# Performance work log

Hardware: AMD Instinct MI355X
Metric: run time of the kernel (lower is better)

The kernel has to match this reference:

```python
import jax, jax.numpy as jnp
import numpy as np

EMB = 128
BINS = 32
CUT = 5.0
NLAYER = 5
NHID = 4  # extra hidden linears in edge MLP (hidden_dim_list has 5 entries total)
N_NODES = 50000
N_EDGES = 800000
N_GRAPH = 256
NODE_CLASS = 100


def setup_inputs() -> dict:
    key = jax.random.key(0)
    ks = jax.random.split(key, 20)
    s = 0.02
    inp = {
        'z': jax.random.randint(ks[0], (N_NODES,), 0, NODE_CLASS),
        'pos': jax.random.normal(ks[1], (N_NODES, 3), dtype=jnp.float32) * 3.0,
        'batch': jnp.sort(jax.random.randint(ks[2], (N_NODES,), 0, N_GRAPH)),
        'edge_index': jax.random.randint(ks[3], (2, N_EDGES), 0, N_NODES),
        # parameters
        'atom_table': jax.random.normal(ks[4], (NODE_CLASS, EMB), dtype=jnp.float32) * s,
        'atom_w': jax.random.normal(ks[5], (EMB, EMB), dtype=jnp.float32) * s,
        'atom_b': jnp.zeros((EMB,), jnp.float32),
        'edge_emb_w': jax.random.normal(ks[6], (BINS, EMB), dtype=jnp.float32) * s,
        'edge_emb_b': jnp.zeros((EMB,), jnp.float32),
        'edge_w0': jax.random.normal(ks[7], (NLAYER, 3 * EMB, EMB), dtype=jnp.float32) * s,
        'edge_b0': jnp.zeros((NLAYER, EMB), jnp.float32),
        'edge_w': jax.random.normal(ks[8], (NLAYER, NHID, EMB, EMB), dtype=jnp.float32) * s,
        'edge_b': jnp.zeros((NLAYER, NHID, EMB), jnp.float32),
        'node_w': jax.random.normal(ks[9], (NLAYER, EMB, EMB), dtype=jnp.float32) * s,
        'node_b': jnp.zeros((NLAYER, EMB), jnp.float32),
        'out_w': jax.random.normal(ks[10], (EMB, 1), dtype=jnp.float32) * s,
        'out_b': jnp.zeros((1,), jnp.float32),
    }
    return inp


def reference(z, pos, batch, edge_index, atom_table, atom_w, atom_b,
              edge_emb_w, edge_emb_b, edge_w0, edge_b0, edge_w, edge_b,
              node_w, node_b, out_w, out_b):
    silu = jax.nn.silu
    row, col = edge_index[0], edge_index[1]

    # atom embedding + linear
    h_node = atom_table[z] @ atom_w + atom_b  # [N, EMB]

    # edge distances -> gaussian basis expansion (linear spacing, log_base=1.0)
    d = jnp.linalg.norm(pos[row] - pos[col], axis=-1)  # [E]
    mu = jnp.linspace(0.0, CUT, BINS, dtype=jnp.float32)
    sigma = CUT / BINS
    basis = jnp.exp(-0.5 * ((d[:, None] - mu) / sigma) ** 2)  # [E, BINS]
    h_edge = basis @ edge_emb_w + edge_emb_b  # [E, EMB]

    # message passing layers
    for l in range(NLAYER):
        m = jnp.concatenate([h_edge, h_node[row], h_node[col]], axis=-1)  # [E, 3*EMB]
        m = silu(m @ edge_w0[l] + edge_b0[l])
        for k in range(NHID):
            m = silu(m @ edge_w[l, k] + edge_b[l, k])
        h_edge = h_edge + m  # residual edge update
        agg = jax.ops.segment_sum(h_edge, row, num_segments=N_NODES)  # [N, EMB]
        h_node = h_node + silu(agg @ node_w[l] + node_b[l])  # residual node update

    # scatter-mean graph pool
    sums = jax.ops.segment_sum(h_node, batch, num_segments=N_GRAPH)
    cnt = jax.ops.segment_sum(jnp.ones((h_node.shape[0],), h_node.dtype), batch, num_segments=N_GRAPH)
    h_graph = sums / jnp.clip(cnt, 1.0)[:, None]

    return h_graph @ out_w + out_b  # [N_GRAPH, 1]
```

## Files before the change

kernel.cpp:

```cpp
#include <hip/hip_runtime.h>

#define EMB      128
#define N_NODES_ 50000
#define N_EDGES_ 800000
#define N_GRAPH_ 256
#define NLAYER_  5

#define WP_ATOM  573440
#define WP_NODE0 589824
#define WP_EMB   671744
#define WP_TOTAL 675840

typedef short short8 __attribute__((ext_vector_type(8)));
typedef float floatx4 __attribute__((ext_vector_type(4)));
typedef unsigned uintx2 __attribute__((ext_vector_type(2)));

__device__ __forceinline__ float silu_f(float x) {
    return __fdividef(x, 1.0f + __expf(-x));
}
__device__ __forceinline__ float bf2f(unsigned short h) {
    return __uint_as_float(((unsigned)h) << 16);
}
__device__ __forceinline__ unsigned short f2bf(float f) {
    unsigned u = __float_as_uint(f);
    unsigned r = 0x7FFFu + ((u >> 16) & 1u);
    return (unsigned short)((u + r) >> 16);
}

#if defined(__has_builtin)
#if __has_builtin(__builtin_amdgcn_cvt_pk_bf16_f32)
#define HAVE_PK_BF16 1
#endif
#if __has_builtin(__builtin_amdgcn_permlane16_swap) && __has_builtin(__builtin_amdgcn_permlane32_swap)
#define HAVE_PERMLANE_SWAP 1
#endif
#endif

#ifdef HAVE_PK_BF16
typedef __bf16 bf16x2 __attribute__((ext_vector_type(2)));
__device__ __forceinline__ unsigned f2bf_pk(float a, float b) {
    bf16x2 v = __builtin_amdgcn_cvt_pk_bf16_f32(a, b);
    unsigned u;
    __builtin_memcpy(&u, &v, 4);
    return u;
}
#else
__device__ __forceinline__ unsigned f2bf_pk(float a, float b) {
    return (unsigned)f2bf(a) | ((unsigned)f2bf(b) << 16);
}
#endif

__device__ __forceinline__ void wave_lds_fence() {
    __builtin_amdgcn_fence(__ATOMIC_ACQ_REL, "wavefront");
    __builtin_amdgcn_wave_barrier();
}

__device__ __forceinline__ void gload_lds16(const unsigned short* g, unsigned short* l) {
    __builtin_amdgcn_global_load_lds(
        (const __attribute__((address_space(1))) void*)g,
        (__attribute__((address_space(3))) void*)l,
        16, 0, 0);
}

__device__ __forceinline__ void swap32(unsigned &a, unsigned &b) {
#ifdef HAVE_PERMLANE_SWAP
    uintx2 r = __builtin_amdgcn_permlane32_swap(a, b, false, false);
    a = r.x; b = r.y;
#else
    const int lane = (int)(threadIdx.x & 63);
    const int idx = (lane ^ 32) << 2;
    const unsigned ta = (unsigned)__builtin_amdgcn_ds_bpermute(idx, (int)a);
    const unsigned tb = (unsigned)__builtin_amdgcn_ds_bpermute(idx, (int)b);
    const bool hi = lane >= 32;
    const unsigned na = hi ? tb : a;
    const unsigned nb = hi ? b : ta;
    a = na; b = nb;
#endif
}
__device__ __forceinline__ void swap16(unsigned &a, unsigned &b) {
#ifdef HAVE_PERMLANE_SWAP
    uintx2 r = __builtin_amdgcn_permlane16_swap(a, b, false, false);
    a = r.x; b = r.y;
#else
    const unsigned ta = (unsigned)__builtin_amdgcn_ds_swizzle((int)a, 0x401F);
    const unsigned tb = (unsigned)__builtin_amdgcn_ds_swizzle((int)b, 0x401F);
    const bool odd = ((threadIdx.x >> 4) & 1) != 0;
    const unsigned na = odd ? tb : a;
    const unsigned nb = odd ? b : ta;
    a = na; b = nb;
#endif
}

__device__ __forceinline__ short8 xchg_frag(uint2 pkE, uint2 pkO) {
    unsigned a0 = pkE.x, b0 = pkO.x;
    unsigned a1 = pkE.y, b1 = pkO.y;
    swap32(a0, b0); swap16(a0, b0);
    swap32(a1, b1); swap16(a1, b1);
    union { short8 s; unsigned u[4]; } r;
    r.u[0] = a0; r.u[1] = a1; r.u[2] = b0; r.u[3] = b1;
    return r.s;
}

__device__ __forceinline__ floatx4 upair_sum(uint2 a, uint2 b) {
    floatx4 r;
    r[0] = bf2f((unsigned short)(a.x & 0xFFFF)) + bf2f((unsigned short)(b.x & 0xFFFF));
    r[1] = bf2f((unsigned short)(a.x >> 16))    + bf2f((unsigned short)(b.x >> 16));
    r[2] = bf2f((unsigned short)(a.y & 0xFFFF)) + bf2f((unsigned short)(b.y & 0xFFFF));
    r[3] = bf2f((unsigned short)(a.y >> 16))    + bf2f((unsigned short)(b.y >> 16));
    return r;
}

__global__ __launch_bounds__(256) void hist_kernel(
    const int* __restrict__ row, int* __restrict__ hist)
{
    const int e = blockIdx.x * 256 + threadIdx.x;
    if (e < N_EDGES_) atomicAdd(&hist[row[e]], 1);
}

__global__ __launch_bounds__(256) void scan_kernel(
    const int* __restrict__ hist, int* __restrict__ cursor)
{
    __shared__ int ssum[256];
    const int tid = threadIdx.x;
    const int chunk = (N_NODES_ + 255) / 256;
    const int base = tid * chunk;
    int s = 0;
    for (int i = 0; i < chunk; ++i) {
        const int idx = base + i;
        if (idx < N_NODES_) s += hist[idx];
    }
    ssum[tid] = s;
    __syncthreads();
    for (int off = 1; off < 256; off <<= 1) {
        const int t2 = (tid >= off) ? ssum[tid - off] : 0;
        __syncthreads();
        ssum[tid] += t2;
        __syncthreads();
    }
    int run = ssum[tid] - s;
    for (int i = 0; i < chunk; ++i) {
        const int idx = base + i;
        if (idx < N_NODES_) { cursor[idx] = run; run += hist[idx]; }
    }
}

__global__ __launch_bounds__(256) void scatter_kernel(
    const int* __restrict__ row, const int* __restrict__ col,
    int* __restrict__ cursor, int* __restrict__ row_s, int* __restrict__ col_s)
{
    const int e = blockIdx.x * 256 + threadIdx.x;
    if (e >= N_EDGES_) return;
    const int r = row[e];
    const int p = atomicAdd(&cursor[r], 1);
    row_s[p] = r;
    col_s[p] = col[e];
}

__global__ __launch_bounds__(256) void pack_w_kernel(
    const float* __restrict__ edge_w0, const float* __restrict__ edge_w,
    const float* __restrict__ atom_w, const float* __restrict__ node_w,
    const float* __restrict__ edge_emb_w,
    unsigned short* __restrict__ Wp)
{
    const int bid = blockIdx.x;
    int Kb, t;
    const float* src;
    unsigned short* dst;
    if (bid < 200) {
        const int l = bid / 40, r = bid % 40, s = r / 8;
        t = r % 8;
        Kb = (s == 0) ? 12 : 4;
        src = (s == 0) ? edge_w0 + (size_t)l * 384 * 128
                       : edge_w + ((size_t)l * 4 + (s - 1)) * 128 * 128;
        dst = Wp + (size_t)l * 114688 + ((s == 0) ? 0 : (49152 + (s - 1) * 16384))
            + (size_t)t * Kb * 512;
    } else if (bid < 208) {
        t = bid - 200; Kb = 4; src = atom_w;
        dst = Wp + WP_ATOM + (size_t)t * Kb * 512;
    } else if (bid < 248) {
        const int l = (bid - 208) >> 3; t = (bid - 208) & 7; Kb = 4;
        src = node_w + (size_t)l * 128 * 128;
        dst = Wp + WP_NODE0 + (size_t)l * 16384 + (size_t)t * Kb * 512;
    } else {
        t = bid - 248; Kb = 1; src = edge_emb_w;
        dst = Wp + WP_EMB + (size_t)t * 512;
    }
    const int n = Kb * 512;
    for (int p = threadIdx.x; p < n; p += 256) {
        const int j = p & 7, lane = (p >> 3) & 63, kb = p >> 9;
        const int k  = kb * 32 + ((lane >> 4) << 3) + j;
        const int nn = t * 16 + (lane & 15);
        dst[p] = f2bf(src[(size_t)k * 128 + nn]);
    }
}

__global__ __launch_bounds__(128, 5) void edge_mlp_csr_kernel(
    unsigned short* __restrict__ h_edge,
    const unsigned short* __restrict__ Ur, const unsigned short* __restrict__ Uc,
    const int* __restrict__ row_s, const int* __restrict__ col_s,
    const unsigned short* __restrict__ Wp, const float* __restrict__ bh)
{
    __shared__ __align__(16) unsigned short Xs[4096];
    __shared__ __align__(16) unsigned short Ys[4096];

    const int tid  = threadIdx.x;
    const int lane = tid & 63;
    const int wv   = tid >> 6;
    const int lr   = lane & 15;
    const int lg   = lane >> 4;
    const int e0   = blockIdx.x * 32;
    const int ntb  = 4 * wv;

    const int srow = 16 * wv + lg;
#pragma unroll
    for (int j = 0; j < 4; ++j) {
        const int r = srow + 4 * j;
        const int c = lr ^ (r & 7);
        gload_lds16(h_edge + (size_t)(e0 + r) * 128 + c * 8,
                    &Xs[(16 * wv + 4 * j) * 128]);
    }

    int rid[2], cid[2];
#pragma unroll
    for (int et = 0; et < 2; ++et) {
        const int e = e0 + et * 16 + lr;
        rid[et] = row_s[e];
        cid[et] = col_s[e];
    }

    floatx4 acc[2][4];
    {
        uint2 gr[2][4], gc[2][4];
#pragma unroll
        for (int et = 0; et < 2; ++et)
#pragma unroll
            for (int n = 0; n < 4; ++n) {
                const int fo = (ntb + n) * 16 + lg * 4;
                gr[et][n] = *(const uint2*)(Ur + (size_t)rid[et] * 128 + fo);
                gc[et][n] = *(const uint2*)(Uc + (size_t)cid[et] * 128 + fo);
            }
#pragma unroll
        for (int et = 0; et < 2; ++et)
#pragma unroll
            for (int n = 0; n < 4; ++n)
                acc[et][n] = upair_sum(gr[et][n], gc[et][n]);
    }

    asm volatile("s_waitcnt vmcnt(0)" ::: "memory");
    __syncthreads();

    short8 he_reg[4];
    const int t_ = tid >> 2, q_ = tid & 3;

#pragma unroll 1
    for (int s = 0; s < 5; ++s) {
        const unsigned short* __restrict__ bin = (s & 1) ? Ys : Xs;
        unsigned short* __restrict__ bout      = (s & 1) ? Xs : Ys;
        const unsigned short* __restrict__ Ws =
            (s == 0) ? Wp : (Wp + 49152 + (size_t)(s - 1) * 16384);
        const int nst = (s == 0) ? 12 : 4;

        if (s >= 1) {
            const float* bias = bh + (size_t)(s - 1) * 128;
#pragma unroll
            for (int n = 0; n < 4; ++n) {
                const float4 bv = *(const float4*)&bias[(ntb + n) * 16 + lg * 4];
                acc[0][n] = (floatx4){bv.x, bv.y, bv.z, bv.w};
                acc[1][n] = acc[0][n];
            }
        }

#pragma unroll 2
        for (int kk = 0; kk < 4; ++kk) {
            short8 wf[4];
#pragma unroll
            for (int n = 0; n < 4; ++n)
                wf[n] = *(const short8*)(Ws + ((size_t)((ntb + n) * nst + kk) * 64 + lane) * 8);
#pragma unroll
            for (int et = 0; et < 2; ++et) {
                const int r = et * 16 + lr;
                const short8 mf = *(const short8*)&bin[r * 128 + (((kk * 4 + lg) ^ (r & 7)) << 3)];
#pragma unroll
                for (int n = 0; n < 4; ++n)
                    acc[et][n] = __builtin_amdgcn_mfma_f32_16x16x32_bf16(wf[n], mf, acc[et][n], 0, 0, 0);
            }
        }

#pragma unroll
        for (int et = 0; et < 2; ++et) {
            const int r = et * 16 + lr;
#pragma unroll
            for (int n = 0; n < 4; ++n) {
                uint2 p;
                p.x = f2bf_pk(silu_f(acc[et][n][0]), silu_f(acc[et][n][1]));
                p.y = f2bf_pk(silu_f(acc[et][n][2]), silu_f(acc[et][n][3]));
                const int c = (2 * (ntb + n) + (lg >> 1)) ^ (r & 7);
                *(uint2*)&bout[r * 128 + c * 8 + (lg & 1) * 4] = p;
            }
        }

        if (s == 0) {
#pragma unroll
            for (int i = 0; i < 4; ++i) {
                const int ch = q_ + 4 * i;
                he_reg[i] = *(const short8*)&Xs[t_ * 128 + ((ch ^ (t_ & 7)) << 3)];
            }
        }
        __syncthreads();
    }

#pragma unroll
    for (int i = 0; i < 4; ++i) {
        const int ch = q_ + 4 * i;
        const short8 mv = *(const short8*)&Ys[t_ * 128 + ((ch ^ (t_ & 7)) << 3)];
        const short8 ov = he_reg[i];
        float v[8];
#pragma unroll
        for (int j = 0; j < 8; ++j)
            v[j] = bf2f((unsigned short)ov[j]) + bf2f((unsigned short)mv[j]);
        uint4 sv;
        sv.x = f2bf_pk(v[0], v[1]);
        sv.y = f2bf_pk(v[2], v[3]);
        sv.z = f2bf_pk(v[4], v[5]);
        sv.w = f2bf_pk(v[6], v[7]);
        *(uint4*)(h_edge + (size_t)(e0 + t_) * 128 + ch * 8) = sv;
    }
}

__global__ __launch_bounds__(256, 3) void node_agg_gemm_kernel(
    const unsigned short* __restrict__ h_edge,
    const int* __restrict__ hist, const int* __restrict__ cur_end,
    const unsigned short* __restrict__ Wpm, const float* __restrict__ bias,
    unsigned short* __restrict__ h_node_bf, int N,
    const unsigned short* __restrict__ Wp0n, const float* __restrict__ b0n,
    unsigned short* __restrict__ Ur, unsigned short* __restrict__ Uc)
{
    __shared__ __align__(16) unsigned short B[64][136];
    const int tid  = threadIdx.x;
    const int lane = tid & 63;
    const int wv   = tid >> 6;
    const int n0   = blockIdx.x * 64;

    {
        const int t = tid >> 2, q = tid & 3;
        const int n = n0 + t;
        float a[32];
#pragma unroll
        for (int j = 0; j < 32; ++j) a[j] = 0.f;
        if (n < N) {
            const int e_end = cur_end[n];
            const int e_beg = e_end - hist[n];
            for (int e = e_beg; e < e_end; ++e) {
                const unsigned short* p = &h_edge[(size_t)e * 128 + q * 32];
#pragma unroll
                for (int g = 0; g < 4; ++g) {
                    const short8 v = *(const short8*)(p + g * 8);
#pragma unroll
                    for (int j = 0; j < 8; ++j)
                        a[g * 8 + j] += bf2f((unsigned short)v[j]);
                }
            }
        }
#pragma unroll
        for (int g = 0; g < 4; ++g) {
            uint4 pk;
            pk.x = f2bf_pk(a[g * 8 + 0], a[g * 8 + 1]);
            pk.y = f2bf_pk(a[g * 8 + 2], a[g * 8 + 3]);
            pk.z = f2bf_pk(a[g * 8 + 4], a[g * 8 + 5]);
            pk.w = f2bf_pk(a[g * 8 + 6], a[g * 8 + 7]);
            *(uint4*)&B[t][q * 32 + g * 8] = pk;
        }
    }
    wave_lds_fence();

    const int lr = lane & 15, lg = lane >> 4;
    floatx4 acc[8];
#pragma unroll
    for (int nt = 0; nt < 8; ++nt) {
        const float4 bv = *(const float4*)&bias[nt * 16 + lg * 4];
        acc[nt] = (floatx4){bv.x, bv.y, bv.z, bv.w};
    }
    const unsigned short* brow = &B[wv * 16 + lr][0];
#pragma unroll 2
    for (int kb = 0; kb < 4; ++kb) {
        const short8 mf = *(const short8*)(brow + kb * 32 + lg * 8);
#pragma unroll
        for (int nt = 0; nt < 8; ++nt) {
            const short8 wf = *(const short8*)(Wpm + ((size_t)(nt * 4 + kb) * 64 + lane) * 8);
            acc[nt] = __builtin_amdgcn_mfma_f32_16x16x32_bf16(wf, mf, acc[nt], 0, 0, 0);
        }
    }
    const int node = n0 + wv * 16 + lr;
    unsigned short* drow = &h_node_bf[(size_t)node * 128];

    uint2 o[8];
#pragma unroll
    for (int nt = 0; nt < 8; ++nt) {
        float x0 = silu_f(acc[nt][0]), x1 = silu_f(acc[nt][1]);
        float x2 = silu_f(acc[nt][2]), x3 = silu_f(acc[nt][3]);
        if (node < N) {
            const uint2 d = *(const uint2*)(drow + nt * 16 + lg * 4);
            x0 += bf2f((unsigned short)(d.x & 0xFFFF));
            x1 += bf2f((unsigned short)(d.x >> 16));
            x2 += bf2f((unsigned short)(d.y & 0xFFFF));
            x3 += bf2f((unsigned short)(d.y >> 16));
        }
        o[nt].x = f2bf_pk(x0, x1);
        o[nt].y = f2bf_pk(x2, x3);
    }
    if (node < N) {
#pragma unroll
        for (int nt = 0; nt < 8; ++nt)
            *(uint2*)(drow + nt * 16 + lg * 4) = o[nt];
    }

    if (Wp0n) {
        short8 bf[4];
#pragma unroll
        for (int kb = 0; kb < 4; ++kb)
            bf[kb] = xchg_frag(o[2 * kb], o[2 * kb + 1]);

        floatx4 au[8];
#pragma unroll
        for (int nt = 0; nt < 8; ++nt) {
            const float4 bv = *(const float4*)&b0n[nt * 16 + lg * 4];
            au[nt] = (floatx4){bv.x, bv.y, bv.z, bv.w};
        }
#pragma unroll 2
        for (int kb = 0; kb < 4; ++kb) {
#pragma unroll
            for (int nt = 0; nt < 8; ++nt) {
                const short8 wr = *(const short8*)(Wp0n + ((size_t)(nt * 12 + 4 + kb) * 64 + lane) * 8);
                au[nt] = __builtin_amdgcn_mfma_f32_16x16x32_bf16(wr, bf[kb], au[nt], 0, 0, 0);
            }
        }
        if (node < N) {
            unsigned short* rrow = Ur + (size_t)node * 128;
#pragma unroll
            for (int nt = 0; nt < 8; ++nt) {
                uint2 u;
                u.x = f2bf_pk(au[nt][0], au[nt][1]);
                u.y = f2bf_pk(au[nt][2], au[nt][3]);
                *(uint2*)(rrow + nt * 16 + lg * 4) = u;
            }
        }
#pragma unroll
        for (int nt = 0; nt < 8; ++nt)
            au[nt] = (floatx4){0.f, 0.f, 0.f, 0.f};
#pragma unroll 2
        for (int kb = 0; kb < 4; ++kb) {
#pragma unroll
            for (int nt = 0; nt < 8; ++nt) {
                const short8 wc = *(const short8*)(Wp0n + ((size_t)(nt * 12 + 8 + kb) * 64 + lane) * 8);
                au[nt] = __builtin_amdgcn_mfma_f32_16x16x32_bf16(wc, bf[kb], au[nt], 0, 0, 0);
            }
        }
        if (node < N) {
            unsigned short* crow = Uc + (size_t)node * 128;
#pragma unroll
            for (int nt = 0; nt < 8; ++nt) {
                uint2 u;
                u.x = f2bf_pk(au[nt][0], au[nt][1]);
                u.y = f2bf_pk(au[nt][2], au[nt][3]);
                *(uint2*)(crow + nt * 16 + lg * 4) = u;
            }
        }
    }
}

__global__ __launch_bounds__(256, 3) void atom_gemm_mfma_kernel(
    const float* __restrict__ src, const int* __restrict__ gidx,
    const unsigned short* __restrict__ Wpm, const float* __restrict__ bias,
    unsigned short* __restrict__ dst, int N,
    const unsigned short* __restrict__ Wp0n, const float* __restrict__ b0n,
    unsigned short* __restrict__ Ur, unsigned short* __restrict__ Uc)
{
    __shared__ __align__(16) unsigned short B[64][136];
    const int tid  = threadIdx.x;
    const int lane = tid & 63;
    const int wv   = tid >> 6;
    const int n0   = blockIdx.x * 64;

    {
        const int t = tid >> 2, q = tid & 3;
        const int node = n0 + t;
        const float* srow = src;
        if (node < N) srow = &src[(size_t)gidx[node] * 128];
#pragma unroll
        for (int i = 0; i < 4; ++i) {
            const int k8 = (q + 4 * i) << 3;
            uint4 pk = make_uint4(0, 0, 0, 0);
            if (node < N) {
                const float4 f0 = *(const float4*)(srow + k8);
                const float4 f1 = *(const float4*)(srow + k8 + 4);
                pk.x = f2bf_pk(f0.x, f0.y);
                pk.y = f2bf_pk(f0.z, f0.w);
                pk.z = f2bf_pk(f1.x, f1.y);
                pk.w = f2bf_pk(f1.z, f1.w);
            }
            *(uint4*)&B[t][k8] = pk;
        }
    }
    wave_lds_fence();

    const int lr = lane & 15, lg = lane >> 4;
    floatx4 acc[8];
#pragma unroll
    for (int nt = 0; nt < 8; ++nt) {
        const float4 bv = *(const float4*)&bias[nt * 16 + lg * 4];
        acc[nt] = (floatx4){bv.x, bv.y, bv.z, bv.w};
    }
    const unsigned short* brow = &B[wv * 16 + lr][0];
#pragma unroll 2
    for (int kb = 0; kb < 4; ++kb) {
        const short8 mf = *(const short8*)(brow + kb * 32 + lg * 8);
#pragma unroll
        for (int nt = 0; nt < 8; ++nt) {
            const short8 wf = *(const short8*)(Wpm + ((size_t)(nt * 4 + kb) * 64 + lane) * 8);
            acc[nt] = __builtin_amdgcn_mfma_f32_16x16x32_bf16(wf, mf, acc[nt], 0, 0, 0);
        }
    }
    const int node = n0 + wv * 16 + lr;
    uint2 o[8];
#pragma unroll
    for (int nt = 0; nt < 8; ++nt) {
        o[nt].x = f2bf_pk(acc[nt][0], acc[nt][1]);
        o[nt].y = f2bf_pk(acc[nt][2], acc[nt][3]);
    }
    if (node < N) {
        unsigned short* drow = &dst[(size_t)node * 128];
#pragma unroll
        for (int nt = 0; nt < 8; ++nt)
            *(uint2*)(drow + nt * 16 + lg * 4) = o[nt];
    }

    {
        short8 bf[4];
#pragma unroll
        for (int kb = 0; kb < 4; ++kb)
            bf[kb] = xchg_frag(o[2 * kb], o[2 * kb + 1]);

        floatx4 au[8];
#pragma unroll
        for (int nt = 0; nt < 8; ++nt) {
            const float4 bv = *(const float4*)&b0n[nt * 16 + lg * 4];
            au[nt] = (floatx4){bv.x, bv.y, bv.z, bv.w};
        }
#pragma unroll 2
        for (int kb = 0; kb < 4; ++kb) {
#pragma unroll
            for (int nt = 0; nt < 8; ++nt) {
                const short8 wr = *(const short8*)(Wp0n + ((size_t)(nt * 12 + 4 + kb) * 64 + lane) * 8);
                au[nt] = __builtin_amdgcn_mfma_f32_16x16x32_bf16(wr, bf[kb], au[nt], 0, 0, 0);
            }
        }
        if (node < N) {
            unsigned short* rrow = Ur + (size_t)node * 128;
#pragma unroll
            for (int nt = 0; nt < 8; ++nt) {
                uint2 u;
                u.x = f2bf_pk(au[nt][0], au[nt][1]);
                u.y = f2bf_pk(au[nt][2], au[nt][3]);
                *(uint2*)(rrow + nt * 16 + lg * 4) = u;
            }
        }
#pragma unroll
        for (int nt = 0; nt < 8; ++nt)
            au[nt] = (floatx4){0.f, 0.f, 0.f, 0.f};
#pragma unroll 2
        for (int kb = 0; kb < 4; ++kb) {
#pragma unroll
            for (int nt = 0; nt < 8; ++nt) {
                const short8 wc = *(const short8*)(Wp0n + ((size_t)(nt * 12 + 8 + kb) * 64 + lane) * 8);
                au[nt] = __builtin_amdgcn_mfma_f32_16x16x32_bf16(wc, bf[kb], au[nt], 0, 0, 0);
            }
        }
        if (node < N) {
            unsigned short* crow = Uc + (size_t)node * 128;
#pragma unroll
            for (int nt = 0; nt < 8; ++nt) {
                uint2 u;
                u.x = f2bf_pk(au[nt][0], au[nt][1]);
                u.y = f2bf_pk(au[nt][2], au[nt][3]);
                *(uint2*)(crow + nt * 16 + lg * 4) = u;
            }
        }
    }
}

__global__ __launch_bounds__(256, 4) void edge_embed_mfma_kernel(
    const float* __restrict__ pos, const int* __restrict__ row, const int* __restrict__ col,
    const unsigned short* __restrict__ Wpe, const float* __restrict__ bemb,
    unsigned short* __restrict__ h_edge)
{
    __shared__ __align__(16) unsigned short Bas[64][40];
    const int tid  = threadIdx.x;
    const int lane = tid & 63;
    const int wv   = tid >> 6;
    const int e0   = blockIdx.x * 64;

    {
        const int t = tid >> 2, q = tid & 3;
        const int rr = row[e0 + t], cc = col[e0 + t];
        const float dx = pos[rr * 3 + 0] - pos[cc * 3 + 0];
        const float dy = pos[rr * 3 + 1] - pos[cc * 3 + 1];
        const float dz = pos[rr * 3 + 2] - pos[cc * 3 + 2];
        const float d = sqrtf(dx * dx + dy * dy + dz * dz);
        const float invs = 32.0f / 5.0f;
        float e[8];
#pragma unroll
        for (int j = 0; j < 8; ++j) {
            const float mu = (float)(q * 8 + j) * (5.0f / 31.0f);
            const float tt = (d - mu) * invs;
            e[j] = __expf(-0.5f * tt * tt);
        }
        uint4 pk;
        pk.x = f2bf_pk(e[0], e[1]);
        pk.y = f2bf_pk(e[2], e[3]);
        pk.z = f2bf_pk(e[4], e[5]);
        pk.w = f2bf_pk(e[6], e[7]);
        *(uint4*)&Bas[t][q * 8] = pk;
    }
    wave_lds_fence();

    const int lr = lane & 15, lg = lane >> 4;
    floatx4 acc[8];
#pragma unroll
    for (int nt = 0; nt < 8; ++nt) {
        const float4 bv = *(const float4*)&bemb[nt * 16 + lg * 4];
        acc[nt] = (floatx4){bv.x, bv.y, bv.z, bv.w};
    }
    const short8 mf = *(const short8*)&Bas[wv * 16 + lr][lg * 8];
#pragma unroll
    for (int nt = 0; nt < 8; ++nt) {
        const short8 wf = *(const short8*)(Wpe + ((size_t)nt * 64 + lane) * 8);
        acc[nt] = __builtin_amdgcn_mfma_f32_16x16x32_bf16(wf, mf, acc[nt], 0, 0, 0);
    }
    unsigned short* erow = &h_edge[(size_t)(e0 + wv * 16 + lr) * 128];
#pragma unroll
    for (int nt = 0; nt < 8; ++nt) {
        uint2 o;
        o.x = f2bf_pk(acc[nt][0], acc[nt][1]);
        o.y = f2bf_pk(acc[nt][2], acc[nt][3]);
        *(uint2*)(erow + nt * 16 + lg * 4) = o;
    }
}

__global__ __launch_bounds__(128) void pool_kernel(
    const unsigned short* __restrict__ h_node_bf, const int* __restrict__ batch,
    float* __restrict__ sums, float* __restrict__ cnt, int N)
{
    __shared__ int bb[256];
    const int tid = threadIdx.x;
    const int n0 = blockIdx.x * 256;
    for (int idx = tid; idx < 256; idx += 128) {
        int n = n0 + idx;
        bb[idx] = (n < N) ? batch[n] : -1;
    }
    __syncthreads();
    int cur = bb[0];
    float run = 0.f, runc = 0.f;
    for (int i = 0; i < 256; ++i) {
        const int b = bb[i];
        if (b < 0) break;
        if (b != cur) {
            atomicAdd(&sums[(size_t)cur * 128 + tid], run);
            if (tid == 0) atomicAdd(&cnt[cur], runc);
            run = 0.f; runc = 0.f; cur = b;
        }
        run += bf2f(h_node_bf[(size_t)(n0 + i) * 128 + tid]);
        runc += 1.f;
    }
    atomicAdd(&sums[(size_t)cur * 128 + tid], run);
    if (tid == 0) atomicAdd(&cnt[cur], runc);
}

__global__ __launch_bounds__(256) void final_kernel(
    const float* __restrict__ sums, const float* __restrict__ cnt,
    const float* __restrict__ out_w, const float* __restrict__ out_b,
    float* __restrict__ out)
{
    const int g = threadIdx.x;
    const float c = fmaxf(cnt[g], 1.0f);
    float acc = 0.f;
    for (int jj = 0; jj < 128; ++jj) acc = fmaf(sums[(size_t)g * 128 + jj], out_w[jj], acc);
    out[g] = acc / c + out_b[0];
}

__global__ void zero_out_kernel(float* out, int n) {
    int i = blockIdx.x * 256 + threadIdx.x;
    if (i < n) out[i] = 0.f;
}


extern "C" void kernel_launch(void* const* d_in, const int* in_sizes, int n_in,
                              void* d_out, int out_size, void* d_ws, size_t ws_size,
                              hipStream_t stream)
{
    const int*   z          = (const int*)  d_in[0];
    const float* pos        = (const float*)d_in[1];
    const int*   batch      = (const int*)  d_in[2];
    const int*   eidx       = (const int*)  d_in[3];
    const float* atom_table = (const float*)d_in[4];
    const float* atom_w     = (const float*)d_in[5];
    const float* atom_b     = (const float*)d_in[6];
    const float* edge_emb_w = (const float*)d_in[7];
    const float* edge_emb_b = (const float*)d_in[8];
    const float* edge_w0    = (const float*)d_in[9];
    const float* edge_b0    = (const float*)d_in[10];
    const float* edge_w     = (const float*)d_in[11];
    const float* edge_b     = (const float*)d_in[12];
    const float* node_w     = (const float*)d_in[13];
    const float* node_b     = (const float*)d_in[14];
    const float* out_w      = (const float*)d_in[15];
    const float* out_b      = (const float*)d_in[16];
    const int* row = eidx;
    const int* col = eidx + N_EDGES_;

    float* aggb = (float*)d_ws;
    float* sums = aggb + (size_t)N_NODES_ * EMB;
    float* cnt  = sums + (size_t)N_GRAPH_ * EMB;
    unsigned short* h_node_bf = (unsigned short*)(cnt + N_GRAPH_);
    unsigned short* h_edge    = h_node_bf + (size_t)N_NODES_ * EMB;
    unsigned short* Wp        = h_edge + (size_t)N_EDGES_ * EMB;
    int* hist   = (int*)(Wp + WP_TOTAL);
    int* cursor = hist + N_NODES_;
    int* row_s  = cursor + N_NODES_;
    int* col_s  = row_s + N_EDGES_;

    unsigned short* Ur = (unsigned short*)aggb;
    unsigned short* Uc = Ur + (size_t)N_NODES_ * EMB;

    const size_t need = ((size_t)(N_NODES_ * EMB + N_GRAPH_ * EMB + N_GRAPH_)) * 4
                      + ((size_t)N_NODES_ * EMB + (size_t)N_EDGES_ * EMB + (size_t)WP_TOTAL) * 2
                      + ((size_t)N_NODES_ * 2 + (size_t)N_EDGES_ * 2) * 4;

    if (ws_size < need) {
        zero_out_kernel<<<1, 256, 0, stream>>>((float*)d_out, N_GRAPH_);
        return;
    }

    const int grid_rows64 = (N_NODES_ + 63) / 64;

    (void)hipMemsetAsync(hist, 0, N_NODES_ * sizeof(int), stream);
    hist_kernel<<<(N_EDGES_ + 255) / 256, 256, 0, stream>>>(row, hist);
    scan_kernel<<<1, 256, 0, stream>>>(hist, cursor);
    scatter_kernel<<<(N_EDGES_ + 255) / 256, 256, 0, stream>>>(row, col, cursor, row_s, col_s);

    pack_w_kernel<<<256, 256, 0, stream>>>(edge_w0, edge_w, atom_w, node_w, edge_emb_w, Wp);

    atom_gemm_mfma_kernel<<<grid_rows64, 256, 0, stream>>>(
        atom_table, z, Wp + WP_ATOM, atom_b, h_node_bf, N_NODES_,
        Wp, edge_b0, Ur, Uc);
    edge_embed_mfma_kernel<<<N_EDGES_ / 64, 256, 0, stream>>>(
        pos, row_s, col_s, Wp + WP_EMB, edge_emb_b, h_edge);

    for (int l = 0; l < NLAYER_; ++l) {
        edge_mlp_csr_kernel<<<N_EDGES_ / 32, 128, 0, stream>>>(
            h_edge, Ur, Uc, row_s, col_s,
            Wp + (size_t)l * 114688,
            edge_b + (size_t)l * 4 * 128);
        const bool last = (l == NLAYER_ - 1);
        node_agg_gemm_kernel<<<grid_rows64, 256, 0, stream>>>(
            h_edge, hist, cursor,
            Wp + WP_NODE0 + (size_t)l * 16384, node_b + (size_t)l * 128,
            h_node_bf, N_NODES_,
            last ? (const unsigned short*)nullptr : (Wp + (size_t)(l + 1) * 114688),
            last ? edge_b0 : (edge_b0 + (size_t)(l + 1) * 128),
            Ur, Uc);
    }

    (void)hipMemsetAsync(sums, 0, ((size_t)N_GRAPH_ * EMB + N_GRAPH_) * sizeof(float), stream);
    pool_kernel<<<(N_NODES_ + 255) / 256, 128, 0, stream>>>(h_node_bf, batch, sums, cnt, N_NODES_);
    final_kernel<<<1, 256, 0, stream>>>(sums, cnt, out_w, out_b, (float*)d_out);
}
```

Baseline: 2.997 ms.

## Double edge tile per block and interleave Ur/Uc node projections into one buffer

The edge MLP kernel now processes 64 edges per 256-thread block instead of 32 per 128-thread block. Each wave owns two output column tiles over all four 16-edge row groups, so each weight fragment loaded is reused across more edges. The row and column node projections are interleaved into a single 256-wide buffer, so each lane fetches one 16-byte chunk per endpoint instead of several 8-byte loads. Layer 0 is peeled out of the loop. In exchange, LDS per block doubles and occupancy may drop under the unchanged min-blocks launch bound.

```diff
diff --git a/kernel.cpp b/kernel.cpp
--- a/kernel.cpp
+++ b/kernel.cpp
@@ -194,22 +194,30 @@
     }
 }
 
-__global__ __launch_bounds__(128, 5) void edge_mlp_csr_kernel(
+__global__ __launch_bounds__(256, 5) void edge_mlp_csr_kernel(
     unsigned short* __restrict__ h_edge,
-    const unsigned short* __restrict__ Ur, const unsigned short* __restrict__ Uc,
+    const unsigned short* __restrict__ UU,
     const int* __restrict__ row_s, const int* __restrict__ col_s,
     const unsigned short* __restrict__ Wp, const float* __restrict__ bh)
 {
-    __shared__ __align__(16) unsigned short Xs[4096];
-    __shared__ __align__(16) unsigned short Ys[4096];
+    __shared__ __align__(16) unsigned short Xs[8192];
+    __shared__ __align__(16) unsigned short Ys[8192];
 
     const int tid  = threadIdx.x;
+    const int e0   = blockIdx.x * 64;
     const int lane = tid & 63;
     const int wv   = tid >> 6;
     const int lr   = lane & 15;
     const int lg   = lane >> 4;
-    const int e0   = blockIdx.x * 32;
-    const int ntb  = 4 * wv;
+    const int nt0  = 2 * wv, nt1 = nt0 + 1;
+
+    int rid[4], cid[4];
+#pragma unroll
+    for (int et = 0; et < 4; ++et) {
+        const int e = e0 + et * 16 + lr;
+        rid[et] = row_s[e];
+        cid[et] = col_s[e];
+    }
 
     const int srow = 16 * wv + lg;
 #pragma unroll
@@ -220,91 +228,107 @@
                     &Xs[(16 * wv + 4 * j) * 128]);
     }
 
-    int rid[2], cid[2];
-#pragma unroll
-    for (int et = 0; et < 2; ++et) {
-        const int e = e0 + et * 16 + lr;
-        rid[et] = row_s[e];
-        cid[et] = col_s[e];
-    }
-
-    floatx4 acc[2][4];
-    {
-        uint2 gr[2][4], gc[2][4];
-#pragma unroll
-        for (int et = 0; et < 2; ++et)
-#pragma unroll
-            for (int n = 0; n < 4; ++n) {
-                const int fo = (ntb + n) * 16 + lg * 4;
-                gr[et][n] = *(const uint2*)(Ur + (size_t)rid[et] * 128 + fo);
-                gc[et][n] = *(const uint2*)(Uc + (size_t)cid[et] * 128 + fo);
-            }
-#pragma unroll
-        for (int et = 0; et < 2; ++et)
-#pragma unroll
-            for (int n = 0; n < 4; ++n)
-                acc[et][n] = upair_sum(gr[et][n], gc[et][n]);
+    const int uoff = lg * 64 + wv * 16;
+    uint4 ur4[4], uc4[4];
+#pragma unroll
+    for (int et = 0; et < 4; ++et) {
+        ur4[et] = *(const uint4*)(UU + (size_t)rid[et] * 256 + uoff);
+        uc4[et] = *(const uint4*)(UU + (size_t)cid[et] * 256 + uoff + 8);
     }
 
     asm volatile("s_waitcnt vmcnt(0)" ::: "memory");
     __syncthreads();
 
+    floatx4 acc0[4], acc1[4];
+#pragma unroll
+    for (int et = 0; et < 4; ++et) {
+        uint2 ra, rb, ca, cb;
+        ra.x = ur4[et].x; ra.y = ur4[et].y;
+        rb.x = ur4[et].z; rb.y = ur4[et].w;
+        ca.x = uc4[et].x; ca.y = uc4[et].y;
+        cb.x = uc4[et].z; cb.y = uc4[et].w;
+        acc0[et] = upair_sum(ra, ca);
+        acc1[et] = upair_sum(rb, cb);
+    }
+
+    const unsigned short* aptr0 = Wp + ((size_t)(nt0 * 12) * 64 + lane) * 8;
+    const unsigned short* aptr1 = Wp + ((size_t)(nt1 * 12) * 64 + lane) * 8;
+#pragma unroll 2
+    for (int kk = 0; kk < 4; ++kk) {
+        const short8 wf0 = *(const short8*)(aptr0 + (size_t)kk * 512);
+        const short8 wf1 = *(const short8*)(aptr1 + (size_t)kk * 512);
+#pragma unroll
+        for (int et = 0; et < 4; ++et) {
+            const int r = et * 16 + lr;
+            const short8 mf = *(const short8*)&Xs[r * 128 + (((kk * 4 + lg) ^ (r & 7)) << 3)];
+            acc0[et] = __builtin_amdgcn_mfma_f32_16x16x32_bf16(wf0, mf, acc0[et], 0, 0, 0);
+            acc1[et] = __builtin_amdgcn_mfma_f32_16x16x32_bf16(wf1, mf, acc1[et], 0, 0, 0);
+        }
+    }
+
+    const int t_ = tid >> 2, q_ = tid & 3;
     short8 he_reg[4];
-    const int t_ = tid >> 2, q_ = tid & 3;
+#pragma unroll
+    for (int i = 0; i < 4; ++i) {
+        const int ch = q_ + 4 * i;
+        he_reg[i] = *(const short8*)&Xs[t_ * 128 + ((ch ^ (t_ & 7)) << 3)];
+    }
+
+#pragma unroll
+    for (int et = 0; et < 4; ++et) {
+        const int r = et * 16 + lr;
+        uint2 p0, p1;
+        p0.x = f2bf_pk(silu_f(acc0[et][0]), silu_f(acc0[et][1]));
+        p0.y = f2bf_pk(silu_f(acc0[et][2]), silu_f(acc0[et][3]));
+        p1.x = f2bf_pk(silu_f(acc1[et][0]), silu_f(acc1[et][1]));
+        p1.y = f2bf_pk(silu_f(acc1[et][2]), silu_f(acc1[et][3]));
+        const int c0 = (2 * nt0 + (lg >> 1)) ^ (r & 7);
+        const int c1 = (2 * nt1 + (lg >> 1)) ^ (r & 7);
+        *(uint2*)&Ys[r * 128 + c0 * 8 + (lg & 1) * 4] = p0;
+        *(uint2*)&Ys[r * 128 + c1 * 8 + (lg & 1) * 4] = p1;
+    }
+    __syncthreads();
 
 #pragma unroll 1
-    for (int s = 0; s < 5; ++s) {
-        const unsigned short* __restrict__ bin = (s & 1) ? Ys : Xs;
-        unsigned short* __restrict__ bout      = (s & 1) ? Xs : Ys;
-        const unsigned short* __restrict__ Ws =
-            (s == 0) ? Wp : (Wp + 49152 + (size_t)(s - 1) * 16384);
-        const int nst = (s == 0) ? 12 : 4;
-
-        if (s >= 1) {
-            const float* bias = bh + (size_t)(s - 1) * 128;
-#pragma unroll
-            for (int n = 0; n < 4; ++n) {
-                const float4 bv = *(const float4*)&bias[(ntb + n) * 16 + lg * 4];
-                acc[0][n] = (floatx4){bv.x, bv.y, bv.z, bv.w};
-                acc[1][n] = acc[0][n];
-            }
-        }
-
+    for (int s = 1; s < 5; ++s) {
+        const unsigned short* bin = (s & 1) ? Ys : Xs;
+        unsigned short* bout      = (s & 1) ? Xs : Ys;
+        const unsigned short* __restrict__ Ws = Wp + 49152 + (size_t)(s - 1) * 16384;
+        const float* __restrict__ bias = bh + (size_t)(s - 1) * 128;
+
+        const float4 bv0 = *(const float4*)&bias[nt0 * 16 + lg * 4];
+        const float4 bv1 = *(const float4*)&bias[nt1 * 16 + lg * 4];
+#pragma unroll
+        for (int et = 0; et < 4; ++et) {
+            acc0[et] = (floatx4){bv0.x, bv0.y, bv0.z, bv0.w};
+            acc1[et] = (floatx4){bv1.x, bv1.y, bv1.z, bv1.w};
+        }
+        const unsigned short* ap0 = Ws + ((size_t)(nt0 * 4) * 64 + lane) * 8;
+        const unsigned short* ap1 = Ws + ((size_t)(nt1 * 4) * 64 + lane) * 8;
 #pragma unroll 2
         for (int kk = 0; kk < 4; ++kk) {
-            short8 wf[4];
-#pragma unroll
-            for (int n = 0; n < 4; ++n)
-                wf[n] = *(const short8*)(Ws + ((size_t)((ntb + n) * nst + kk) * 64 + lane) * 8);
-#pragma unroll
-            for (int et = 0; et < 2; ++et) {
+            const short8 wf0 = *(const short8*)(ap0 + (size_t)kk * 512);
+            const short8 wf1 = *(const short8*)(ap1 + (size_t)kk * 512);
+#pragma unroll
+            for (int et = 0; et < 4; ++et) {
                 const int r = et * 16 + lr;
                 const short8 mf = *(const short8*)&bin[r * 128 + (((kk * 4 + lg) ^ (r & 7)) << 3)];
-#pragma unroll
-                for (int n = 0; n < 4; ++n)
-                    acc[et][n] = __builtin_amdgcn_mfma_f32_16x16x32_bf16(wf[n], mf, acc[et][n], 0, 0, 0);
-            }
-        }
-
-#pragma unroll
-        for (int et = 0; et < 2; ++et) {
+                acc0[et] = __builtin_amdgcn_mfma_f32_16x16x32_bf16(wf0, mf, acc0[et], 0, 0, 0);
+                acc1[et] = __builtin_amdgcn_mfma_f32_16x16x32_bf16(wf1, mf, acc1[et], 0, 0, 0);
+            }
+        }
+#pragma unroll
+        for (int et = 0; et < 4; ++et) {
             const int r = et * 16 + lr;
-#pragma unroll
-            for (int n = 0; n < 4; ++n) {
-                uint2 p;
-                p.x = f2bf_pk(silu_f(acc[et][n][0]), silu_f(acc[et][n][1]));
-                p.y = f2bf_pk(silu_f(acc[et][n][2]), silu_f(acc[et][n][3]));
-                const int c = (2 * (ntb + n) + (lg >> 1)) ^ (r & 7);
-                *(uint2*)&bout[r * 128 + c * 8 + (lg & 1) * 4] = p;
-            }
-        }
-
-        if (s == 0) {
-#pragma unroll
-            for (int i = 0; i < 4; ++i) {
-                const int ch = q_ + 4 * i;
-                he_reg[i] = *(const short8*)&Xs[t_ * 128 + ((ch ^ (t_ & 7)) << 3)];
-            }
+            uint2 p0, p1;
+            p0.x = f2bf_pk(silu_f(acc0[et][0]), silu_f(acc0[et][1]));
+            p0.y = f2bf_pk(silu_f(acc0[et][2]), silu_f(acc0[et][3]));
+            p1.x = f2bf_pk(silu_f(acc1[et][0]), silu_f(acc1[et][1]));
+            p1.y = f2bf_pk(silu_f(acc1[et][2]), silu_f(acc1[et][3]));
+            const int c0 = (2 * nt0 + (lg >> 1)) ^ (r & 7);
+            const int c1 = (2 * nt1 + (lg >> 1)) ^ (r & 7);
+            *(uint2*)&bout[r * 128 + c0 * 8 + (lg & 1) * 4] = p0;
+            *(uint2*)&bout[r * 128 + c1 * 8 + (lg & 1) * 4] = p1;
         }
         __syncthreads();
     }
@@ -333,7 +357,7 @@
     const unsigned short* __restrict__ Wpm, const float* __restrict__ bias,
     unsigned short* __restrict__ h_node_bf, int N,
     const unsigned short* __restrict__ Wp0n, const float* __restrict__ b0n,
-    unsigned short* __restrict__ Ur, unsigned short* __restrict__ Uc)
+    unsigned short* __restrict__ UU)
 {
     __shared__ __align__(16) unsigned short B[64][136];
     const int tid  = threadIdx.x;
@@ -435,13 +459,13 @@
             }
         }
         if (node < N) {
-            unsigned short* rrow = Ur + (size_t)node * 128;
+            unsigned short* urow = UU + (size_t)node * 256;
 #pragma unroll
             for (int nt = 0; nt < 8; ++nt) {
                 uint2 u;
                 u.x = f2bf_pk(au[nt][0], au[nt][1]);
                 u.y = f2bf_pk(au[nt][2], au[nt][3]);
-                *(uint2*)(rrow + nt * 16 + lg * 4) = u;
+                *(uint2*)(urow + lg * 64 + (nt >> 1) * 16 + (nt & 1) * 4) = u;
             }
         }
 #pragma unroll
@@ -456,13 +480,13 @@
             }
         }
         if (node < N) {
-            unsigned short* crow = Uc + (size_t)node * 128;
+            unsigned short* urow = UU + (size_t)node * 256;
 #pragma unroll
             for (int nt = 0; nt < 8; ++nt) {
                 uint2 u;
                 u.x = f2bf_pk(au[nt][0], au[nt][1]);
                 u.y = f2bf_pk(au[nt][2], au[nt][3]);
-                *(uint2*)(crow + nt * 16 + lg * 4) = u;
+                *(uint2*)(urow + lg * 64 + (nt >> 1) * 16 + (nt & 1) * 4 + 8) = u;
             }
         }
     }
@@ -473,7 +497,7 @@
     const unsigned short* __restrict__ Wpm, const float* __restrict__ bias,
     unsigned short* __restrict__ dst, int N,
     const unsigned short* __restrict__ Wp0n, const float* __restrict__ b0n,
-    unsigned short* __restrict__ Ur, unsigned short* __restrict__ Uc)
+    unsigned short* __restrict__ UU)
 {
     __shared__ __align__(16) unsigned short B[64][136];
     const int tid  = threadIdx.x;
@@ -555,13 +579,13 @@
             }
         }
         if (node < N) {
-            unsigned short* rrow = Ur + (size_t)node * 128;
+            unsigned short* urow = UU + (size_t)node * 256;
 #pragma unroll
             for (int nt = 0; nt < 8; ++nt) {
                 uint2 u;
                 u.x = f2bf_pk(au[nt][0], au[nt][1]);
                 u.y = f2bf_pk(au[nt][2], au[nt][3]);
-                *(uint2*)(rrow + nt * 16 + lg * 4) = u;
+                *(uint2*)(urow + lg * 64 + (nt >> 1) * 16 + (nt & 1) * 4) = u;
             }
         }
 #pragma unroll
@@ -576,13 +600,13 @@
             }
         }
         if (node < N) {
-            unsigned short* crow = Uc + (size_t)node * 128;
+            unsigned short* urow = UU + (size_t)node * 256;
 #pragma unroll
             for (int nt = 0; nt < 8; ++nt) {
                 uint2 u;
                 u.x = f2bf_pk(au[nt][0], au[nt][1]);
                 u.y = f2bf_pk(au[nt][2], au[nt][3]);
-                *(uint2*)(crow + nt * 16 + lg * 4) = u;
+                *(uint2*)(urow + lg * 64 + (nt >> 1) * 16 + (nt & 1) * 4 + 8) = u;
             }
         }
     }
@@ -728,8 +752,7 @@
     int* row_s  = cursor + N_NODES_;
     int* col_s  = row_s + N_EDGES_;
 
-    unsigned short* Ur = (unsigned short*)aggb;
-    unsigned short* Uc = Ur + (size_t)N_NODES_ * EMB;
+    unsigned short* UU = (unsigned short*)aggb;
 
     const size_t need = ((size_t)(N_NODES_ * EMB + N_GRAPH_ * EMB + N_GRAPH_)) * 4
                       + ((size_t)N_NODES_ * EMB + (size_t)N_EDGES_ * EMB + (size_t)WP_TOTAL) * 2
@@ -751,13 +774,13 @@
 
     atom_gemm_mfma_kernel<<<grid_rows64, 256, 0, stream>>>(
         atom_table, z, Wp + WP_ATOM, atom_b, h_node_bf, N_NODES_,
-        Wp, edge_b0, Ur, Uc);
+        Wp, edge_b0, UU);
     edge_embed_mfma_kernel<<<N_EDGES_ / 64, 256, 0, stream>>>(
         pos, row_s, col_s, Wp + WP_EMB, edge_emb_b, h_edge);
 
     for (int l = 0; l < NLAYER_; ++l) {
-        edge_mlp_csr_kernel<<<N_EDGES_ / 32, 128, 0, stream>>>(
-            h_edge, Ur, Uc, row_s, col_s,
+        edge_mlp_csr_kernel<<<N_EDGES_ / 64, 256, 0, stream>>>(
+            h_edge, UU, row_s, col_s,
             Wp + (size_t)l * 114688,
             edge_b + (size_t)l * 4 * 128);
         const bool last = (l == NLAYER_ - 1);
@@ -767,7 +790,7 @@
             h_node_bf, N_NODES_,
             last ? (const unsigned short*)nullptr : (Wp + (size_t)(l + 1) * 114688),
             last ? edge_b0 : (edge_b0 + (size_t)(l + 1) * 128),
-            Ur, Uc);
+            UU);
     }
 
     (void)hipMemsetAsync(sums, 0, ((size_t)N_GRAPH_ * EMB + N_GRAPH_) * sizeof(float), stream);
```

Measured after the change: 2.748 ms. -8.3%, faster.
